# Kernel optimization log

Hardware: AMD Instinct MI355X
Metric: run time of the kernel (lower is better)

The kernel has to match this reference:

```python
import jax, jax.numpy as jnp
import numpy as np

FEAT_DIM = 128  # used for the 1/sqrt(2*feat_dim) attention scale, per the source
_DN = ('NCHW', 'OIHW', 'NCHW')


def _conv_block(x, w1, b1, w2, b2):
    # Conv2d(k=3, stride=1, pad=0) -> ReLU -> Conv2d(k=3) -> ReLU
    h = jax.lax.conv_general_dilated(x, w1, (1, 1), 'VALID', dimension_numbers=_DN)
    h = jax.nn.relu(h + b1[None, :, None, None])
    h = jax.lax.conv_general_dilated(h, w2, (1, 1), 'VALID', dimension_numbers=_DN)
    return jax.nn.relu(h + b2[None, :, None, None])


def setup_inputs() -> dict:
    key = jax.random.key(0)
    ks = jax.random.split(key, 16)
    E, C, H, W = 2048, 16, 16, 16
    G, N = 16, 128  # 16 graphs x 128 edges
    fd = FEAT_DIM
    edge_feat = jax.random.normal(ks[0], (E, C, H, W), dtype=jnp.float32)
    edge_graph_id = (jnp.arange(E) // N).astype(jnp.int64)  # sorted, equal-size groups

    def conv_w(k, out_c, in_c):
        std = 1.0 / np.sqrt(in_c * 9)
        return jax.random.normal(k, (out_c, in_c, 3, 3), dtype=jnp.float32) * std

    inp = {'edge_feat': edge_feat, 'edge_graph_id': edge_graph_id}
    i = 1
    for name in ('q', 'k', 'v'):
        inp[f'{name}_w1'] = conv_w(ks[i], fd, C)
        inp[f'{name}_b1'] = jnp.zeros((fd,), dtype=jnp.float32)
        inp[f'{name}_w2'] = conv_w(ks[i + 1], fd, fd)
        inp[f'{name}_b2'] = jnp.zeros((fd,), dtype=jnp.float32)
        i += 2
    return inp


def reference(edge_feat, edge_graph_id,
              q_w1, q_b1, q_w2, q_b2,
              k_w1, k_b1, k_w2, k_b2,
              v_w1, v_b1, v_w2, v_b2):
    q = _conv_block(edge_feat, q_w1, q_b1, q_w2, q_b2)  # [E, 128, 12, 12]
    k = _conv_block(edge_feat, k_w1, k_b1, k_w2, k_b2)
    v = _conv_block(edge_feat, v_w1, v_b1, v_w2, v_b2)
    E = q.shape[0]
    feat_shape = q.shape[-3:]
    G = int(edge_graph_id[-1]) + 1  # sorted contiguous equal-size groups
    D = feat_shape[0] * feat_shape[1] * feat_shape[2]
    qf = q.reshape(G, E // G, D)
    kf = k.reshape(G, E // G, D)
    vf = v.reshape(G, E // G, D)
    scale = 1.0 / np.sqrt(2 * FEAT_DIM).astype(np.float32)
    attn = jax.nn.softmax(jnp.einsum('gnd,gmd->gnm', qf, kf) * scale, axis=-1)
    out = jnp.einsum('gnm,gmd->gnd', attn, vf)
    return out.reshape(E, *feat_shape)
```

## Files before the change

kernel.cpp:

```cpp
#include <hip/hip_runtime.h>
#include <hip/hip_bf16.h>

typedef unsigned short u16;
typedef unsigned int   u32;

typedef __bf16 bf16x8 __attribute__((ext_vector_type(8)));
typedef float  f32x4  __attribute__((ext_vector_type(4)));

struct alignas(16) US8  { u16 s[8]; };
struct alignas(8)  US4  { u16 s[4]; };
struct alignas(16) UI4  { u32 d[4]; };
struct alignas(8)  U32x2{ u32 x, y; };

__device__ __forceinline__ u16 f2bf(float f) {
  u32 x = __builtin_bit_cast(u32, f);
  return (u16)((x + 0x7fffu + ((x >> 16) & 1u)) >> 16);
}
__device__ __forceinline__ u32 cvtpk(float a, float b) {
  u32 r;
  asm("v_cvt_pk_bf16_f32 %0, %1, %2" : "=v"(r) : "v"(a), "v"(b));
  return r;
}
__device__ __forceinline__ bf16x8 ld8(const u16* p) {
  return __builtin_bit_cast(bf16x8, *(const US8*)p);
}
__device__ __forceinline__ f32x4 mfma16(bf16x8 a, bf16x8 b, f32x4 c) {
  return __builtin_amdgcn_mfma_f32_16x16x32_bf16(a, b, c, 0, 0, 0);
}
__device__ __forceinline__ f32x4 zero4() { f32x4 z; z[0]=0.f; z[1]=0.f; z[2]=0.f; z[3]=0.f; return z; }

#define NE     2048
#define DFULL  18432
#define XROW   24

__global__ void prep_weights(const float* __restrict__ w1q, const float* __restrict__ w1k, const float* __restrict__ w1v,
                             const float* __restrict__ w2q, const float* __restrict__ w2k, const float* __restrict__ w2v,
                             u16* __restrict__ w1p, u16* __restrict__ w2p)
{
  int idx = blockIdx.x * blockDim.x + threadIdx.x;
  int stride = gridDim.x * blockDim.x;
  for (int i = idx; i < 3*128*160; i += stride) {
    int b = i / (128*160); int r = i % (128*160);
    int oc = r / 160, k = r % 160;
    u16 v = 0;
    if (k < 144) {
      int kk = k >> 4, ic = k & 15;
      const float* w = (b == 0) ? w1q : (b == 1) ? w1k : w1v;
      v = f2bf(w[oc*144 + ic*9 + kk]);
    }
    w1p[i] = v;
  }
  for (int i = idx; i < 3*128*1152; i += stride) {
    int b = i / (128*1152); int r = i % (128*1152);
    int oc = r / 1152, k = r % 1152;
    int kk = k >> 7, ic = k & 127;
    const float* w = (b == 0) ? w2q : (b == 1) ? w2k : w2v;
    w2p[i] = f2bf(w[oc*1152 + ic*9 + kk]);
  }
}

__global__ __launch_bounds__(256, 2)
void conv_fused(const float* __restrict__ edge_feat,
                const u16* __restrict__ w1p, const u16* __restrict__ w2p,
                const float* __restrict__ b1q, const float* __restrict__ b1k, const float* __restrict__ b1v,
                const float* __restrict__ b2q, const float* __restrict__ b2k, const float* __restrict__ b2v,
                u16* __restrict__ outq, u16* __restrict__ outk, u16* __restrict__ outv)
{
  const int bb = blockIdx.x / NE;
  const int e  = blockIdx.x % NE;
  const int t = threadIdx.x;
  const int w = t >> 6, l = t & 63;
  const int l15 = l & 15, lq = l >> 4;

  __shared__ __align__(16) u16 x_hwc[256*XROW + 8];
  __shared__ __align__(16) u16 h1t[196 * 128];
  __shared__ float b1f[128], b2f[128];

  {
    const float* xin = edge_feat + (size_t)e * 4096 + t;
    float v[16];
    #pragma unroll
    for (int c = 0; c < 16; ++c) v[c] = xin[c*256];
    UI4 lo_, hi_;
    #pragma unroll
    for (int i = 0; i < 4; ++i) lo_.d[i] = cvtpk(v[2*i],   v[2*i+1]);
    #pragma unroll
    for (int i = 0; i < 4; ++i) hi_.d[i] = cvtpk(v[8+2*i], v[8+2*i+1]);
    *(UI4*)(x_hwc + t*XROW)     = lo_;
    *(UI4*)(x_hwc + t*XROW + 8) = hi_;
  }
  {
    const float* b1p = bb == 0 ? b1q : bb == 1 ? b1k : b1v;
    const float* b2p = bb == 0 ? b2q : bb == 1 ? b2k : b2v;
    if (t < 128) { b1f[t] = b1p[t]; b2f[t] = b2p[t]; }
    if (t < 8) x_hwc[256*XROW + t] = 0;
  }
  __syncthreads();

  const u16* W1b = w1p + bb * (128*160);
  f32x4 acc1[2][13];
  #pragma unroll
  for (int mi = 0; mi < 2; ++mi)
    #pragma unroll
    for (int nt = 0; nt < 13; ++nt) acc1[mi][nt] = zero4();

  int offb[13];
  #pragma unroll
  for (int nt = 0; nt < 13; ++nt) {
    int p = nt*16 + l15; if (p > 195) p = 195;
    int y = p / 14, x = p % 14;
    offb[nt] = (y*16 + x) * (XROW*2);
  }

  #pragma unroll
  for (int ks = 0; ks < 5; ++ks) {
    int k = ks*32 + lq*8;
    bf16x8 a0 = ld8(W1b + ((w*2 + 0)*16 + l15)*160 + k);
    bf16x8 a1 = ld8(W1b + ((w*2 + 1)*16 + l15)*160 + k);
    int kk = k >> 4;
    int ky = kk / 3, kx = kk - ky*3;
    int koffB = (ky*16 + kx)*(XROW*2) + (k & 15)*2;
    bool kvalid = (k < 144);
    #pragma unroll
    for (int nt = 0; nt < 13; ++nt) {
      int byte = kvalid ? (offb[nt] + koffB) : (256*XROW*2);
      bf16x8 bf = ld8((const u16*)((const char*)x_hwc + byte));
      acc1[0][nt] = mfma16(a0, bf, acc1[0][nt]);
      acc1[1][nt] = mfma16(a1, bf, acc1[1][nt]);
    }
  }

  {
    int oc0 = lq*4;
    #pragma unroll
    for (int mi = 0; mi < 2; ++mi) {
      int ocb = (w*2 + mi)*16 + oc0;
      #pragma unroll
      for (int nt = 0; nt < 13; ++nt) {
        int p = nt*16 + l15;
        if (p < 196) {
          float r0 = acc1[mi][nt][0] + b1f[ocb+0]; r0 = r0 > 0.f ? r0 : 0.f;
          float r1 = acc1[mi][nt][1] + b1f[ocb+1]; r1 = r1 > 0.f ? r1 : 0.f;
          float r2 = acc1[mi][nt][2] + b1f[ocb+2]; r2 = r2 > 0.f ? r2 : 0.f;
          float r3 = acc1[mi][nt][3] + b1f[ocb+3]; r3 = r3 > 0.f ? r3 : 0.f;
          U32x2 val{ cvtpk(r0, r1), cvtpk(r2, r3) };
          int byte = p*256 + ((ocb*2) ^ ((p & 7) << 4));
          *(U32x2*)((char*)h1t + byte) = val;
        }
      }
    }
  }
  __syncthreads();

  int ppb[9], p2o[9];
  #pragma unroll
  for (int nt = 0; nt < 9; ++nt) {
    int y2, x2;
    if (nt < 6) { y2 = nt + 6*(l15 >> 3); x2 = l15 & 7; }
    else        { y2 = (nt-6)*4 + (l15 >> 2); x2 = 8 + (l15 & 3); }
    ppb[nt] = y2*14 + x2;
    p2o[nt] = y2*12 + x2;
  }

  const u16* W2b = w2p + bb * (128*1152);
  f32x4 acc2[2][9];
  #pragma unroll
  for (int mi = 0; mi < 2; ++mi)
    #pragma unroll
    for (int nt = 0; nt < 9; ++nt) acc2[mi][nt] = zero4();

  const u16* A0p = W2b + ((w*2 + 0)*16 + l15)*1152;
  const u16* A1p = W2b + ((w*2 + 1)*16 + l15)*1152;
  bf16x8 a0 = ld8(A0p + lq*8);
  bf16x8 a1 = ld8(A1p + lq*8);
  int lq16 = lq*16;

  #pragma unroll
  for (int kk = 0; kk < 9; ++kk) {
    int ky = kk / 3, kx = kk - ky*3;
    int pkp = ky*14 + kx;
    int ax[9];
    #pragma unroll
    for (int nt = 0; nt < 9; ++nt) {
      int pp = ppb[nt] + pkp;
      ax[nt] = pp*256 + (lq16 ^ ((pp & 7) << 4));
    }
    #pragma unroll
    for (int s = 0; s < 4; ++s) {
      int ks = kk*4 + s;
      int k = ks*32 + lq*8;
      int kn = (ks < 35) ? (k + 32) : (lq*8);
      bf16x8 na0 = ld8(A0p + kn);
      bf16x8 na1 = ld8(A1p + kn);
      int kx6 = s << 6;
      #pragma unroll
      for (int nt = 0; nt < 9; ++nt) {
        bf16x8 bfr = ld8((const u16*)((const char*)h1t + (ax[nt] ^ kx6)));
        acc2[0][nt] = mfma16(a0, bfr, acc2[0][nt]);
        acc2[1][nt] = mfma16(a1, bfr, acc2[1][nt]);
      }
      a0 = na0; a1 = na1;
    }
  }

  u16* outp = bb == 0 ? outq : bb == 1 ? outk : outv;
  u16* oe = outp + (size_t)e * DFULL;
  #pragma unroll
  for (int mi = 0; mi < 2; ++mi) {
    int ocb = (w*2 + mi)*16 + lq*4;
    #pragma unroll
    for (int nt = 0; nt < 9; ++nt) {
      #pragma unroll
      for (int r = 0; r < 4; ++r) {
        float v = acc2[mi][nt][r] + b2f[ocb + r];
        v = v > 0.f ? v : 0.f;
        oe[(ocb + r)*144 + p2o[nt]] = f2bf(v);
      }
    }
  }
}

__global__ __launch_bounds__(256, 2)
void qk_partial(const u16* __restrict__ Q, const u16* __restrict__ K, float* __restrict__ Sp, int nc)
{
  const int g = blockIdx.x / nc, kc = blockIdx.x % nc;
  const int t = threadIdx.x, w = t >> 6, l = t & 63;
  const int l15 = l & 15, lq = l >> 4;
  const int CH = DFULL / nc;
  const u16* Qb = Q + (size_t)g*128*DFULL + kc*CH;
  const u16* Kb = K + (size_t)g*128*DFULL + kc*CH;

  f32x4 acc[2][8];
  #pragma unroll
  for (int mi = 0; mi < 2; ++mi)
    #pragma unroll
    for (int nt = 0; nt < 8; ++nt) acc[mi][nt] = zero4();

  for (int ks = 0; ks < CH/32; ++ks) {
    int k = ks*32 + lq*8;
    bf16x8 a0 = ld8(Qb + (size_t)((w*2 + 0)*16 + l15)*DFULL + k);
    bf16x8 a1 = ld8(Qb + (size_t)((w*2 + 1)*16 + l15)*DFULL + k);
    #pragma unroll
    for (int nt = 0; nt < 8; ++nt) {
      bf16x8 b = ld8(Kb + (size_t)(nt*16 + l15)*DFULL + k);
      acc[0][nt] = mfma16(a0, b, acc[0][nt]);
      acc[1][nt] = mfma16(a1, b, acc[1][nt]);
    }
  }

  float* So = Sp + (size_t)(g*nc + kc)*16384;
  #pragma unroll
  for (int mi = 0; mi < 2; ++mi)
    #pragma unroll
    for (int nt = 0; nt < 8; ++nt) {
      int col = nt*16 + l15;
      #pragma unroll
      for (int r = 0; r < 4; ++r) {
        int row = (w*2 + mi)*16 + lq*4 + r;
        So[row*128 + col] = acc[mi][nt][r];
      }
    }
}

__global__ void softmax_p(const float* __restrict__ Sp, u16* __restrict__ P, int nc)
{
  const int rr = blockIdx.x;
  const int g = rr >> 7, n = rr & 127;
  const int l = threadIdx.x;
  const float* base = Sp + (size_t)g*nc*16384 + n*128;
  float v0 = 0.f, v1 = 0.f;
  for (int kc = 0; kc < nc; ++kc) {
    v0 += base[(size_t)kc*16384 + l];
    v1 += base[(size_t)kc*16384 + 64 + l];
  }
  v0 *= 0.0625f; v1 *= 0.0625f;
  float m = fmaxf(v0, v1);
  #pragma unroll
  for (int s = 32; s; s >>= 1) m = fmaxf(m, __shfl_xor(m, s));
  float e0 = __expf(v0 - m), e1 = __expf(v1 - m);
  float sum = e0 + e1;
  #pragma unroll
  for (int s = 32; s; s >>= 1) sum += __shfl_xor(sum, s);
  float inv = 1.f / sum;
  u16* Pr = P + (size_t)g*16384 + n*128;
  Pr[l]      = f2bf(e0 * inv);
  Pr[64 + l] = f2bf(e1 * inv);
}

__global__ __launch_bounds__(256, 2)
void pv_kernel(const u16* __restrict__ P, const u16* __restrict__ V, float* __restrict__ O)
{
  const int g  = blockIdx.x / 96;
  const int dc = blockIdx.x % 96;
  const int d0 = dc * 192;
  const int t = threadIdx.x, w = t >> 6, l = t & 63;
  const int l15 = l & 15, lq = l >> 4;

  __shared__ __align__(16) u16 Vl[128 * 196];

  const u16* Vg = V + (size_t)g*128*DFULL + d0;
  for (int i = t; i < 6144; i += 256) {
    int m = i / 48, c4 = (i % 48) * 4;
    *(US4*)(Vl + m*196 + c4) = *(const US4*)(Vg + (size_t)m*DFULL + c4);
  }
  __syncthreads();

  const u16* Pg = P + (size_t)g*16384;
  f32x4 acc[2][12];
  #pragma unroll
  for (int mi = 0; mi < 2; ++mi)
    #pragma unroll
    for (int nt = 0; nt < 12; ++nt) acc[mi][nt] = zero4();

  #pragma unroll
  for (int ks = 0; ks < 4; ++ks) {
    int k = ks*32 + lq*8;
    bf16x8 a0 = ld8(Pg + ((w*2 + 0)*16 + l15)*128 + k);
    bf16x8 a1 = ld8(Pg + ((w*2 + 1)*16 + l15)*128 + k);
    #pragma unroll
    for (int nt = 0; nt < 12; ++nt) {
      int d = nt*16 + l15;
      US8 tmp;
      #pragma unroll
      for (int j = 0; j < 8; ++j) tmp.s[j] = Vl[(k + j)*196 + d];
      bf16x8 b = __builtin_bit_cast(bf16x8, tmp);
      acc[0][nt] = mfma16(a0, b, acc[0][nt]);
      acc[1][nt] = mfma16(a1, b, acc[1][nt]);
    }
  }

  float* Og = O + (size_t)g*128*DFULL + d0;
  #pragma unroll
  for (int mi = 0; mi < 2; ++mi)
    #pragma unroll
    for (int nt = 0; nt < 12; ++nt) {
      int d = nt*16 + l15;
      #pragma unroll
      for (int r = 0; r < 4; ++r) {
        int n = (w*2 + mi)*16 + lq*4 + r;
        Og[(size_t)n*DFULL + d] = acc[mi][nt][r];
      }
    }
}

extern "C" void kernel_launch(void* const* d_in, const int* in_sizes, int n_in,
                              void* d_out, int out_size, void* d_ws, size_t ws_size,
                              hipStream_t stream)
{
  const float* edge_feat = (const float*)d_in[0];
  const float* qw1 = (const float*)d_in[2];
  const float* qb1 = (const float*)d_in[3];
  const float* qw2 = (const float*)d_in[4];
  const float* qb2 = (const float*)d_in[5];
  const float* kw1 = (const float*)d_in[6];
  const float* kb1 = (const float*)d_in[7];
  const float* kw2 = (const float*)d_in[8];
  const float* kb2 = (const float*)d_in[9];
  const float* vw1 = (const float*)d_in[10];
  const float* vb1 = (const float*)d_in[11];
  const float* vw2 = (const float*)d_in[12];
  const float* vb2 = (const float*)d_in[13];

  u16* Qd = (u16*)d_out;
  u16* Kd = (u16*)d_out + (size_t)NE*DFULL;

  char* ws = (char*)d_ws;
  u16*   W1p = (u16*)  (ws + 0);
  u16*   W2p = (u16*)  (ws + 122880);
  u16*   Vb  = (u16*)  (ws + 1007616);
  float* Sp  = (float*)(ws + 76505088);
  int nc = 16;
  size_t need16 = 76505088ull + (size_t)16*16*16384*4 + 524288;
  if (ws_size < need16) nc = 8;
  u16* P = (u16*)(ws + 76505088 + (size_t)16*nc*16384*4);

  prep_weights<<<240, 256, 0, stream>>>(qw1, kw1, vw1, qw2, kw2, vw2, W1p, W2p);
  conv_fused<<<3*NE, 256, 0, stream>>>(edge_feat, W1p, W2p,
                                       qb1, kb1, vb1, qb2, kb2, vb2,
                                       Qd, Kd, Vb);
  qk_partial<<<16*nc, 256, 0, stream>>>(Qd, Kd, Sp, nc);
  softmax_p<<<2048, 64, 0, stream>>>(Sp, P, nc);
  pv_kernel<<<16*96, 256, 0, stream>>>(P, Vb, (float*)d_out);
}
```

Baseline: 427.3 us.

## Retile conv2 MFMA loop as 2x2 warp grid and change h1 LDS swizzle

```diff
diff --git a/kernel.cpp b/kernel.cpp
--- a/kernel.cpp
+++ b/kernel.cpp
@@ -32,6 +32,7 @@
 #define NE     2048
 #define DFULL  18432
 #define XROW   24
+#define H1SWZ(p) ((((p) >> 1) & 3) << 6)
 
 __global__ void prep_weights(const float* __restrict__ w1q, const float* __restrict__ w1k, const float* __restrict__ w1v,
                              const float* __restrict__ w2q, const float* __restrict__ w2k, const float* __restrict__ w2v,
@@ -144,7 +145,7 @@
           float r2 = acc1[mi][nt][2] + b1f[ocb+2]; r2 = r2 > 0.f ? r2 : 0.f;
           float r3 = acc1[mi][nt][3] + b1f[ocb+3]; r3 = r3 > 0.f ? r3 : 0.f;
           U32x2 val{ cvtpk(r0, r1), cvtpk(r2, r3) };
-          int byte = p*256 + ((ocb*2) ^ ((p & 7) << 4));
+          int byte = p*256 + ((ocb*2) ^ H1SWZ(p));
           *(U32x2*)((char*)h1t + byte) = val;
         }
       }
@@ -152,69 +153,82 @@
   }
   __syncthreads();
 
-  int ppb[9], p2o[9];
-  #pragma unroll
-  for (int nt = 0; nt < 9; ++nt) {
+  const int wm = w >> 1, wn = w & 1;
+  const int NT0 = wn ? 5 : 0;
+  const int NTN = wn ? 4 : 5;
+
+  int ppb[5], p2o[5];
+  #pragma unroll
+  for (int i = 0; i < 5; ++i) {
+    int nt = NT0 + i; if (nt > 8) nt = 8;
     int y2, x2;
     if (nt < 6) { y2 = nt + 6*(l15 >> 3); x2 = l15 & 7; }
     else        { y2 = (nt-6)*4 + (l15 >> 2); x2 = 8 + (l15 & 3); }
-    ppb[nt] = y2*14 + x2;
-    p2o[nt] = y2*12 + x2;
+    ppb[i] = y2*14 + x2;
+    p2o[i] = y2*12 + x2;
   }
 
   const u16* W2b = w2p + bb * (128*1152);
-  f32x4 acc2[2][9];
-  #pragma unroll
-  for (int mi = 0; mi < 2; ++mi)
-    #pragma unroll
-    for (int nt = 0; nt < 9; ++nt) acc2[mi][nt] = zero4();
-
-  const u16* A0p = W2b + ((w*2 + 0)*16 + l15)*1152;
-  const u16* A1p = W2b + ((w*2 + 1)*16 + l15)*1152;
-  bf16x8 a0 = ld8(A0p + lq*8);
-  bf16x8 a1 = ld8(A1p + lq*8);
-  int lq16 = lq*16;
+  f32x4 acc2[4][5];
+  #pragma unroll
+  for (int j = 0; j < 4; ++j)
+    #pragma unroll
+    for (int i = 0; i < 5; ++i) acc2[j][i] = zero4();
+
+  const u16* Ap[4];
+  #pragma unroll
+  for (int j = 0; j < 4; ++j) Ap[j] = W2b + ((wm*4 + j)*16 + l15)*1152;
+  bf16x8 a[4], na[4];
+  #pragma unroll
+  for (int j = 0; j < 4; ++j) a[j] = ld8(Ap[j] + lq*8);
+  const int lq16 = lq*16;
 
   #pragma unroll
   for (int kk = 0; kk < 9; ++kk) {
     int ky = kk / 3, kx = kk - ky*3;
     int pkp = ky*14 + kx;
-    int ax[9];
-    #pragma unroll
-    for (int nt = 0; nt < 9; ++nt) {
-      int pp = ppb[nt] + pkp;
-      ax[nt] = pp*256 + (lq16 ^ ((pp & 7) << 4));
+    int ax[5];
+    #pragma unroll
+    for (int i = 0; i < 5; ++i) {
+      int pp = ppb[i] + pkp;
+      ax[i] = pp*256 + (lq16 | H1SWZ(pp));
     }
     #pragma unroll
     for (int s = 0; s < 4; ++s) {
       int ks = kk*4 + s;
       int k = ks*32 + lq*8;
       int kn = (ks < 35) ? (k + 32) : (lq*8);
-      bf16x8 na0 = ld8(A0p + kn);
-      bf16x8 na1 = ld8(A1p + kn);
+      #pragma unroll
+      for (int j = 0; j < 4; ++j) na[j] = ld8(Ap[j] + kn);
       int kx6 = s << 6;
       #pragma unroll
-      for (int nt = 0; nt < 9; ++nt) {
-        bf16x8 bfr = ld8((const u16*)((const char*)h1t + (ax[nt] ^ kx6)));
-        acc2[0][nt] = mfma16(a0, bfr, acc2[0][nt]);
-        acc2[1][nt] = mfma16(a1, bfr, acc2[1][nt]);
-      }
-      a0 = na0; a1 = na1;
+      for (int i = 0; i < 5; ++i) {
+        if (i < NTN) {
+          bf16x8 bfr = ld8((const u16*)((const char*)h1t + (ax[i] ^ kx6)));
+          #pragma unroll
+          for (int j = 0; j < 4; ++j)
+            acc2[j][i] = mfma16(a[j], bfr, acc2[j][i]);
+        }
+      }
+      #pragma unroll
+      for (int j = 0; j < 4; ++j) a[j] = na[j];
     }
   }
 
   u16* outp = bb == 0 ? outq : bb == 1 ? outk : outv;
   u16* oe = outp + (size_t)e * DFULL;
   #pragma unroll
-  for (int mi = 0; mi < 2; ++mi) {
-    int ocb = (w*2 + mi)*16 + lq*4;
-    #pragma unroll
-    for (int nt = 0; nt < 9; ++nt) {
-      #pragma unroll
-      for (int r = 0; r < 4; ++r) {
-        float v = acc2[mi][nt][r] + b2f[ocb + r];
-        v = v > 0.f ? v : 0.f;
-        oe[(ocb + r)*144 + p2o[nt]] = f2bf(v);
+  for (int j = 0; j < 4; ++j) {
+    int ocb = (wm*4 + j)*16 + lq*4;
+    #pragma unroll
+    for (int i = 0; i < 5; ++i) {
+      if (i < NTN) {
+        #pragma unroll
+        for (int r = 0; r < 4; ++r) {
+          float v = acc2[j][i][r] + b2f[ocb + r];
+          v = v > 0.f ? v : 0.f;
+          oe[(ocb + r)*144 + p2o[i]] = f2bf(v);
+        }
       }
     }
   }
```

Result: slower. 583.8 us (+36.6%).
